# Kernel optimization log

Measured on AMD Instinct MI355X. Metric: run time of the kernel, lower is better.

## Reference

```python
import jax, jax.numpy as jnp
import numpy as np

B, N, D, H, F = 16, 257, 1024, 16, 4096
HD = D // H
EPS = 1e-5
GATING_TEMP = 0.25  # gating_hyperparam for steep_sigmoid
SCALE = HD ** -0.5


def layer_norm(x, g, b):
    mu = jnp.mean(x, axis=-1, keepdims=True)
    var = jnp.mean(jnp.square(x - mu), axis=-1, keepdims=True)
    return (x - mu) * jax.lax.rsqrt(var + EPS) * g + b


def quick_gelu(x):
    return x * jax.nn.sigmoid(1.702 * x)


def setup_inputs() -> dict:
    key = jax.random.key(0)
    ks = jax.random.split(key, 24)
    s = 0.02
    inp = {
        'hidden_states': jax.random.normal(ks[0], (B, N, D), jnp.float32),
        'cached_hidden': jax.random.normal(ks[1], (B, N, D), jnp.float32),
        'cached_q': jax.random.normal(ks[2], (B, N, D), jnp.float32),
        'cached_k': jax.random.normal(ks[3], (B, N, D), jnp.float32),
        'cached_v': jax.random.normal(ks[4], (B, N, D), jnp.float32),
        'ln1_g': jnp.ones((D,), jnp.float32),
        'ln1_b': jnp.zeros((D,), jnp.float32),
        'wq': jax.random.normal(ks[5], (D, D), jnp.float32) * s,
        'bq': jnp.zeros((D,), jnp.float32),
        'wk': jax.random.normal(ks[6], (D, D), jnp.float32) * s,
        'bk': jnp.zeros((D,), jnp.float32),
        'wv': jax.random.normal(ks[7], (D, D), jnp.float32) * s,
        'bv': jnp.zeros((D,), jnp.float32),
        'wo': jax.random.normal(ks[8], (D, D), jnp.float32) * s,
        'bo': jnp.zeros((D,), jnp.float32),
        'ln2_g': jnp.ones((D,), jnp.float32),
        'ln2_b': jnp.zeros((D,), jnp.float32),
        'w1': jax.random.normal(ks[9], (D, F), jnp.float32) * s,
        'b1': jnp.zeros((F,), jnp.float32),
        'w2': jax.random.normal(ks[10], (F, D), jnp.float32) * s,
        'b2': jnp.zeros((D,), jnp.float32),
        'threshold': jnp.float32(0.5),
    }
    return inp


def reference(hidden_states, cached_hidden, cached_q, cached_k, cached_v,
              ln1_g, ln1_b, wq, bq, wk, bk, wv, bv, wo, bo,
              ln2_g, ln2_b, w1, b1, w2, b2, threshold):
    # layer_norm1 + QKV projection (layer_norm1_qkv_projection)
    h_ln = layer_norm(hidden_states, ln1_g, ln1_b)
    q = h_ln @ wq + bq
    k = h_ln @ wk + bk
    v = h_ln @ wv + bv

    # reuse module: cosine^1 similarity vs cached hidden, steep_sigmoid gating
    # against learned threshold; soft gather/scatter blend of cached states.
    num = jnp.sum(cached_hidden * hidden_states, axis=-1)           # [B,N]
    den = (jnp.linalg.norm(cached_hidden, axis=-1)
           * jnp.linalg.norm(hidden_states, axis=-1) + 1e-8)
    sim = num / den                                                 # [B,N]
    gate = jax.nn.sigmoid((sim - threshold) / GATING_TEMP)[..., None]  # [B,N,1]

    hidden = gate * cached_hidden + (1.0 - gate) * hidden_states
    q = gate * cached_q + (1.0 - gate) * q
    k = gate * cached_k + (1.0 - gate) * k
    v = gate * cached_v + (1.0 - gate) * v

    # manual bmm-softmax-bmm attention
    qh = (q * SCALE).reshape(B, N, H, HD).transpose(0, 2, 1, 3)  # [B,H,N,hd]
    kh = k.reshape(B, N, H, HD).transpose(0, 2, 1, 3)
    vh = v.reshape(B, N, H, HD).transpose(0, 2, 1, 3)
    scores = jnp.einsum('bhqd,bhkd->bhqk', qh, kh)
    probs = jax.nn.softmax(scores, axis=-1)
    attn = jnp.einsum('bhqk,bhkd->bhqd', probs, vh)
    attn = attn.transpose(0, 2, 1, 3).reshape(B, N, D)
    attn = attn @ wo + bo

    hidden = hidden + attn
    residual = hidden
    hidden = layer_norm(hidden, ln2_g, ln2_b)
    hidden = quick_gelu(hidden @ w1 + b1) @ w2 + b2
    return residual + hidden
```

## Files before the change

### kernel.cpp

```cpp
#include <hip/hip_runtime.h>
#include <hip/hip_bf16.h>
#include <stdint.h>

#define BB   16
#define SEQ  257
#define DD   1024
#define NH   16
#define HD_  64
#define FF   4096
#define MM   (BB*SEQ)
#define MPAD2 4352
#define SPAD 272
#define VPAD 288
#define SCALE_Q 0.125f

typedef __bf16 bf16x8 __attribute__((ext_vector_type(8)));
typedef float  f32x4  __attribute__((ext_vector_type(4)));
typedef unsigned short u16;

__device__ __forceinline__ u16 f2bf(float f) {
  uint32_t u = __float_as_uint(f);
  uint32_t r = (u + 0x7FFFu + ((u >> 16) & 1u)) >> 16;
  return (u16)r;
}
__device__ __forceinline__ float bf2f(u16 u) {
  return __uint_as_float(((uint32_t)u) << 16);
}
__device__ __forceinline__ void gll16(const void* g, void* l) {
  __builtin_amdgcn_global_load_lds(
      (const __attribute__((address_space(1))) void*)g,
      (__attribute__((address_space(3))) void*)l, 16, 0, 0);
}
__device__ __forceinline__ float wsum(float v) {
  #pragma unroll
  for (int o = 1; o < 64; o <<= 1) v += __shfl_xor(v, o);
  return v;
}

__global__ __launch_bounds__(256) void transpose_all(
    const float* __restrict__ wq, const float* __restrict__ wk,
    const float* __restrict__ wv, const float* __restrict__ wo,
    const float* __restrict__ w1, const float* __restrict__ w2,
    u16* __restrict__ wqkvT, u16* __restrict__ woT,
    u16* __restrict__ w1T, u16* __restrict__ w2T) {
  __shared__ float tile[64][65];
  const int bid = blockIdx.x;
  const float* src;  u16* dst;  int R, C, b;
  if (bid < 768)       { int s = bid >> 8;  b = bid & 255;
                         src = s==0?wq:(s==1?wk:wv);  dst = wqkvT + s*1024*1024;
                         R = 1024; C = 1024; }
  else if (bid < 1024) { src = wo;  dst = woT;  b = bid - 768;   R = 1024; C = 1024; }
  else if (bid < 2048) { src = w1;  dst = w1T;  b = bid - 1024;  R = 1024; C = 4096; }
  else                 { src = w2;  dst = w2T;  b = bid - 2048;  R = 4096; C = 1024; }
  const int ctiles = C >> 6;
  const int r0 = (b / ctiles) << 6, c0 = (b % ctiles) << 6;
  const int tx = threadIdx.x & 63, ty = threadIdx.x >> 6;
  #pragma unroll
  for (int it = 0; it < 16; ++it) {
    int rr = it * 4 + ty;
    tile[rr][tx] = src[(size_t)(r0 + rr) * C + c0 + tx];
  }
  __syncthreads();
  #pragma unroll
  for (int it = 0; it < 16; ++it) {
    int rr = it * 4 + ty;
    dst[(size_t)(c0 + rr) * R + r0 + tx] = f2bf(tile[tx][rr]);
  }
}

__global__ __launch_bounds__(256) void vtrans_kernel(
    const u16* __restrict__ vb, u16* __restrict__ vt) {
  __shared__ u16 tile[64][72];
  const int bh = blockIdx.x, c = blockIdx.y;
  const int tx = threadIdx.x & 63, ty = threadIdx.x >> 6;
  const u16* src = vb + (size_t)bh * SPAD * HD_;
  u16* dst = vt + (size_t)bh * HD_ * VPAD;
  #pragma unroll
  for (int it = 0; it < 16; ++it) {
    int r = it * 4 + ty;
    int nn = c * 64 + r;  int nnc = nn < SPAD ? nn : SPAD - 1;
    tile[r][tx] = src[(size_t)nnc * HD_ + tx];
  }
  __syncthreads();
  #pragma unroll
  for (int it = 0; it < 16; ++it) {
    int hd = it * 4 + ty;
    int col = c * 64 + tx;
    if (col < VPAD) dst[(size_t)hd * VPAD + col] = tile[tx][hd];
  }
}

__global__ __launch_bounds__(256) void ln1_gate_kernel(
    const float* __restrict__ h, const float* __restrict__ c,
    const float* __restrict__ g, const float* __restrict__ bta,
    const float* __restrict__ thr, u16* __restrict__ hln,
    float* __restrict__ hblend, float* __restrict__ gate) {
  int m = blockIdx.x, t = threadIdx.x, l = t & 63, w = t >> 6;
  const float4 hv = *(const float4*)(h + (size_t)m * DD + t * 4);
  const float4 cv = *(const float4*)(c + (size_t)m * DD + t * 4);
  float sh = hv.x + hv.y + hv.z + hv.w;
  float sh2 = hv.x*hv.x + hv.y*hv.y + hv.z*hv.z + hv.w*hv.w;
  float sch = hv.x*cv.x + hv.y*cv.y + hv.z*cv.z + hv.w*cv.w;
  float sc2 = cv.x*cv.x + cv.y*cv.y + cv.z*cv.z + cv.w*cv.w;
  sh = wsum(sh); sh2 = wsum(sh2); sch = wsum(sch); sc2 = wsum(sc2);
  __shared__ float red[4][4];
  if (l == 0) { red[w][0]=sh; red[w][1]=sh2; red[w][2]=sch; red[w][3]=sc2; }
  __syncthreads();
  float Sh  = red[0][0]+red[1][0]+red[2][0]+red[3][0];
  float Sh2 = red[0][1]+red[1][1]+red[2][1]+red[3][1];
  float Sch = red[0][2]+red[1][2]+red[2][2]+red[3][2];
  float Sc2 = red[0][3]+red[1][3]+red[2][3]+red[3][3];
  float mean = Sh * (1.f/DD);
  float var  = Sh2 * (1.f/DD) - mean*mean;
  float rs   = rsqrtf(var + 1e-5f);
  float sim  = Sch / (sqrtf(Sc2)*sqrtf(Sh2) + 1e-8f);
  float gv   = 1.f / (1.f + __expf(-(sim - thr[0]) * 4.0f));
  float4 gg = *(const float4*)(g + t*4);
  float4 bb = *(const float4*)(bta + t*4);
  ushort4 ob;
  ob.x = f2bf((hv.x-mean)*rs*gg.x + bb.x);
  ob.y = f2bf((hv.y-mean)*rs*gg.y + bb.y);
  ob.z = f2bf((hv.z-mean)*rs*gg.z + bb.z);
  ob.w = f2bf((hv.w-mean)*rs*gg.w + bb.w);
  *(ushort4*)(hln + (size_t)m * DD + t * 4) = ob;
  float4 hb;
  hb.x = gv*cv.x + (1.f-gv)*hv.x;  hb.y = gv*cv.y + (1.f-gv)*hv.y;
  hb.z = gv*cv.z + (1.f-gv)*hv.z;  hb.w = gv*cv.w + (1.f-gv)*hv.w;
  *(float4*)(hblend + (size_t)m * DD + t * 4) = hb;
  if (t == 0) gate[m] = gv;
}

__global__ __launch_bounds__(256) void ln2_kernel(
    const float* __restrict__ in, const float* __restrict__ g,
    const float* __restrict__ bta, u16* __restrict__ outb) {
  int m = blockIdx.x, t = threadIdx.x, l = t & 63, w = t >> 6;
  const float4 hv = *(const float4*)(in + (size_t)m * DD + t * 4);
  float sh = hv.x + hv.y + hv.z + hv.w;
  float sh2 = hv.x*hv.x + hv.y*hv.y + hv.z*hv.z + hv.w*hv.w;
  sh = wsum(sh); sh2 = wsum(sh2);
  __shared__ float red[4][2];
  if (l == 0) { red[w][0] = sh; red[w][1] = sh2; }
  __syncthreads();
  float Sh  = red[0][0]+red[1][0]+red[2][0]+red[3][0];
  float Sh2 = red[0][1]+red[1][1]+red[2][1]+red[3][1];
  float mean = Sh * (1.f/DD);
  float rs = rsqrtf(Sh2 * (1.f/DD) - mean*mean + 1e-5f);
  float4 gg = *(const float4*)(g + t*4);
  float4 bb = *(const float4*)(bta + t*4);
  ushort4 ob;
  ob.x = f2bf((hv.x-mean)*rs*gg.x + bb.x);
  ob.y = f2bf((hv.y-mean)*rs*gg.y + bb.y);
  ob.z = f2bf((hv.z-mean)*rs*gg.z + bb.z);
  ob.w = f2bf((hv.w-mean)*rs*gg.w + bb.w);
  *(ushort4*)(outb + (size_t)m * DD + t * 4) = ob;
}

template<int EPI>
__global__ __launch_bounds__(256) void gemm_bt(
    const u16* __restrict__ A, const u16* __restrict__ Bt,
    int Kstride, int Kiter,
    const float* __restrict__ bias,
    const float* __restrict__ gate,
    const float* __restrict__ c0, const float* __restrict__ c1, const float* __restrict__ c2,
    const float* __restrict__ bq, const float* __restrict__ bk, const float* __restrict__ bv,
    u16* __restrict__ qb, u16* __restrict__ kb, u16* __restrict__ vb,
    const float* __restrict__ addsrc, float* __restrict__ outf,
    u16* __restrict__ outb, u16* __restrict__ partb) {
  const int tid = threadIdx.x, w = tid >> 6, l = tid & 63, lr = l & 15, lh = l >> 4;
  const int Mt = gridDim.x;
  const int f = blockIdx.y * Mt + blockIdx.x;
  const int nwg = Mt * gridDim.y;
  const int swz = (f & 7) * (nwg >> 3) + (f >> 3);
  const int m0 = (swz % Mt) * 128, n0 = (swz / Mt) * 128;
  const int kBase = blockIdx.z * Kiter;
  const int wm = w >> 1, wn = w & 1;
  __shared__ u16 sA[2][4096], sB[2][4096];
  f32x4 acc[4][4];
  f32x4 zero = {0.f, 0.f, 0.f, 0.f};
  #pragma unroll
  for (int i = 0; i < 4; ++i)
    #pragma unroll
    for (int j = 0; j < 4; ++j) acc[i][j] = zero;

  const int r0 = tid >> 2, cc = (tid & 3) * 8;
  const u16* ga0 = A  + (size_t)(m0 + r0) * Kstride + kBase + cc;
  const u16* ga1 = A  + (size_t)(m0 + 64 + r0) * Kstride + kBase + cc;
  const u16* gb0 = Bt + (size_t)(n0 + r0) * Kstride + kBase + cc;
  const u16* gb1 = Bt + (size_t)(n0 + 64 + r0) * Kstride + kBase + cc;

  const int nt = Kiter >> 5;
  gll16(ga0, &sA[0][w*512]);  gll16(ga1, &sA[0][2048 + w*512]);
  gll16(gb0, &sB[0][w*512]);  gll16(gb1, &sB[0][2048 + w*512]);

  for (int t = 0; t < nt; ++t) {
    const int cur = t & 1;
    __syncthreads();
    if (t + 1 < nt) {
      const int k0 = (t + 1) << 5;
      gll16(ga0 + k0, &sA[cur^1][w*512]);  gll16(ga1 + k0, &sA[cur^1][2048 + w*512]);
      gll16(gb0 + k0, &sB[cur^1][w*512]);  gll16(gb1 + k0, &sB[cur^1][2048 + w*512]);
    }
    bf16x8 af[4], bfr[4];
    #pragma unroll
    for (int mi = 0; mi < 4; ++mi)
      af[mi] = *(const bf16x8*)&sA[cur][(wm*64 + mi*16 + lr)*32 + lh*8];
    #pragma unroll
    for (int ni = 0; ni < 4; ++ni)
      bfr[ni] = *(const bf16x8*)&sB[cur][(wn*64 + ni*16 + lr)*32 + lh*8];
    #pragma unroll
    for (int mi = 0; mi < 4; ++mi)
      #pragma unroll
      for (int ni = 0; ni < 4; ++ni)
        acc[mi][ni] = __builtin_amdgcn_mfma_f32_16x16x32_bf16(af[mi], bfr[ni], acc[mi][ni], 0, 0, 0);
  }

  if constexpr (EPI == 0) {
    const int which = n0 >> 10;
    const float* cb = which==0 ? bq : (which==1 ? bk : bv);
    const float* cp = which==0 ? c0 : (which==1 ? c1 : c2);
    u16* dst = which==0 ? qb : (which==1 ? kb : vb);
    const float scl = which==0 ? SCALE_Q : 1.0f;
    #pragma unroll
    for (int mi = 0; mi < 4; ++mi) {
      #pragma unroll
      for (int r = 0; r < 4; ++r) {
        const int row = m0 + wm*64 + mi*16 + lh*4 + r;
        if (row < MM) {
          const float gv = gate[row];
          const int bidx = row / SEQ, nn = row - bidx * SEQ;
          #pragma unroll
          for (int ni = 0; ni < 4; ++ni) {
            const int col = n0 + wn*64 + ni*16 + lr;
            const int d = col & 1023, hd = d & 63, hh = d >> 6;
            const float lin = acc[mi][ni][r] + cb[d];
            const float val = (gv * cp[(size_t)row*DD + d] + (1.f - gv) * lin) * scl;
            dst[((size_t)(bidx*NH + hh)*SPAD + nn)*HD_ + hd] = f2bf(val);
          }
        }
      }
    }
  } else if constexpr (EPI == 1) {
    #pragma unroll
    for (int mi = 0; mi < 4; ++mi)
      #pragma unroll
      for (int r = 0; r < 4; ++r) {
        const int row = m0 + wm*64 + mi*16 + lh*4 + r;
        if (row < MM) {
          #pragma unroll
          for (int ni = 0; ni < 4; ++ni) {
            const int col = n0 + wn*64 + ni*16 + lr;
            outf[(size_t)row*DD + col] = acc[mi][ni][r] + bias[col] + addsrc[(size_t)row*DD + col];
          }
        }
      }
  } else if constexpr (EPI == 2) {
    #pragma unroll
    for (int mi = 0; mi < 4; ++mi)
      #pragma unroll
      for (int r = 0; r < 4; ++r) {
        const int row = m0 + wm*64 + mi*16 + lh*4 + r;
        if (row < MM) {
          #pragma unroll
          for (int ni = 0; ni < 4; ++ni) {
            const int col = n0 + wn*64 + ni*16 + lr;
            const float x = acc[mi][ni][r] + bias[col];
            const float s = 1.f / (1.f + __expf(-1.702f * x));
            outb[(size_t)row*FF + col] = f2bf(x * s);
          }
        }
      }
  } else {
    u16* pp = partb + (size_t)blockIdx.z * ((size_t)MPAD2 * 1024);
    #pragma unroll
    for (int mi = 0; mi < 4; ++mi)
      #pragma unroll
      for (int r = 0; r < 4; ++r) {
        const int row = m0 + wm*64 + mi*16 + lh*4 + r;
        if (row < MM) {
          #pragma unroll
          for (int ni = 0; ni < 4; ++ni) {
            const int col = n0 + wn*64 + ni*16 + lr;
            pp[(size_t)row*1024 + col] = f2bf(acc[mi][ni][r]);
          }
        }
      }
  }
}

__global__ __launch_bounds__(256) void reduce_mlp2(
    const u16* __restrict__ parts, const float* __restrict__ bias,
    const float* __restrict__ resid, float* __restrict__ out) {
  const size_t PS = (size_t)MPAD2 * 1024;
  const int row = blockIdx.x, t = threadIdx.x, c = t * 4;
  const size_t base = (size_t)row * 1024 + c;
  float4 r = *(const float4*)(resid + base);
  float4 b = *(const float4*)(bias + c);
  float o0 = r.x + b.x, o1 = r.y + b.y, o2 = r.z + b.z, o3 = r.w + b.w;
  #pragma unroll
  for (int p = 0; p < 2; ++p) {
    ushort4 u = *(const ushort4*)(parts + p*PS + base);
    o0 += bf2f(u.x);  o1 += bf2f(u.y);  o2 += bf2f(u.z);  o3 += bf2f(u.w);
  }
  float4 o;  o.x = o0;  o.y = o1;  o.z = o2;  o.w = o3;
  *(float4*)(out + base) = o;
}

__global__ __launch_bounds__(256) void attn_kernel(
    const u16* __restrict__ qb, const u16* __restrict__ kb,
    const u16* __restrict__ vt, u16* __restrict__ attn_out) {
  __shared__ u16 P[64 * 296];
  const int bh = blockIdx.x, b = bh >> 4, hh = bh & 15;
  const int q0 = blockIdx.y * 64;
  const int tid = threadIdx.x, w = tid >> 6, l = tid & 63, lr = l & 15, lh = l >> 4;
  const u16* qp = qb + (size_t)bh * SPAD * HD_;
  const u16* kp = kb + (size_t)bh * SPAD * HD_;
  const u16* vp = vt + (size_t)bh * HD_ * VPAD;

  const int qr = q0 + w*16 + lr;
  const int qrc = qr < 271 ? qr : 271;
  bf16x8 aq0 = *(const bf16x8*)(qp + (size_t)qrc*HD_ + lh*8);
  bf16x8 aq1 = *(const bf16x8*)(qp + (size_t)qrc*HD_ + 32 + lh*8);

  f32x4 st[18];
  f32x4 zero = {0.f,0.f,0.f,0.f};
  #pragma unroll
  for (int t = 0; t < 18; ++t) st[t] = zero;
  #pragma unroll
  for (int t = 0; t < 18; ++t) {
    int key = t*16 + lr;  int keyc = key < 271 ? key : 271;
    bf16x8 b0 = *(const bf16x8*)(kp + (size_t)keyc*HD_ + lh*8);
    bf16x8 b1 = *(const bf16x8*)(kp + (size_t)keyc*HD_ + 32 + lh*8);
    st[t] = __builtin_amdgcn_mfma_f32_16x16x32_bf16(aq0, b0, st[t], 0, 0, 0);
    st[t] = __builtin_amdgcn_mfma_f32_16x16x32_bf16(aq1, b1, st[t], 0, 0, 0);
  }
  #pragma unroll
  for (int t = 0; t < 18; ++t) {
    int key = t*16 + lr;
    if (key >= SEQ) { st[t][0]=-1e30f; st[t][1]=-1e30f; st[t][2]=-1e30f; st[t][3]=-1e30f; }
  }
  float mr[4], sr[4];
  #pragma unroll
  for (int r = 0; r < 4; ++r) {
    float m = st[0][r];
    #pragma unroll
    for (int t = 1; t < 18; ++t) m = fmaxf(m, st[t][r]);
    m = fmaxf(m, __shfl_xor(m, 1));  m = fmaxf(m, __shfl_xor(m, 2));
    m = fmaxf(m, __shfl_xor(m, 4));  m = fmaxf(m, __shfl_xor(m, 8));
    mr[r] = m;  sr[r] = 0.f;
  }
  #pragma unroll
  for (int t = 0; t < 18; ++t)
    #pragma unroll
    for (int r = 0; r < 4; ++r) {
      float p = __expf(st[t][r] - mr[r]);
      st[t][r] = p;  sr[r] += p;
    }
  #pragma unroll
  for (int r = 0; r < 4; ++r) {
    sr[r] += __shfl_xor(sr[r], 1);  sr[r] += __shfl_xor(sr[r], 2);
    sr[r] += __shfl_xor(sr[r], 4);  sr[r] += __shfl_xor(sr[r], 8);
  }
  #pragma unroll
  for (int t = 0; t < 18; ++t)
    #pragma unroll
    for (int r = 0; r < 4; ++r)
      P[(w*16 + lh*4 + r)*296 + t*16 + lr] = f2bf(st[t][r]);
  __syncthreads();

  f32x4 o[4];
  #pragma unroll
  for (int ni = 0; ni < 4; ++ni) o[ni] = zero;
  #pragma unroll
  for (int ks = 0; ks < 9; ++ks) {
    bf16x8 pa = *(const bf16x8*)&P[(w*16 + lr)*296 + ks*32 + lh*8];
    #pragma unroll
    for (int ni = 0; ni < 4; ++ni) {
      bf16x8 bv_ = *(const bf16x8*)(vp + (size_t)(ni*16 + lr)*VPAD + ks*32 + lh*8);
      o[ni] = __builtin_amdgcn_mfma_f32_16x16x32_bf16(pa, bv_, o[ni], 0, 0, 0);
    }
  }
  #pragma unroll
  for (int r = 0; r < 4; ++r) {
    const int qrow = q0 + w*16 + lh*4 + r;
    if (qrow < SEQ) {
      const float inv = 1.f / sr[r];
      #pragma unroll
      for (int ni = 0; ni < 4; ++ni)
        attn_out[(size_t)(b*SEQ + qrow)*DD + hh*HD_ + ni*16 + lr] = f2bf(o[ni][r] * inv);
    }
  }
}

extern "C" void kernel_launch(void* const* d_in, const int* in_sizes, int n_in,
                              void* d_out, int out_size, void* d_ws, size_t ws_size,
                              hipStream_t stream) {
  (void)in_sizes; (void)n_in; (void)out_size; (void)ws_size;
  const float* hidden   = (const float*)d_in[0];
  const float* cached_h = (const float*)d_in[1];
  const float* cached_q = (const float*)d_in[2];
  const float* cached_k = (const float*)d_in[3];
  const float* cached_v = (const float*)d_in[4];
  const float* ln1_g = (const float*)d_in[5];
  const float* ln1_b = (const float*)d_in[6];
  const float* wq = (const float*)d_in[7];
  const float* bq = (const float*)d_in[8];
  const float* wk = (const float*)d_in[9];
  const float* bk = (const float*)d_in[10];
  const float* wv = (const float*)d_in[11];
  const float* bv = (const float*)d_in[12];
  const float* wo = (const float*)d_in[13];
  const float* bo = (const float*)d_in[14];
  const float* ln2_g = (const float*)d_in[15];
  const float* ln2_b = (const float*)d_in[16];
  const float* w1 = (const float*)d_in[17];
  const float* b1 = (const float*)d_in[18];
  const float* w2 = (const float*)d_in[19];
  const float* b2 = (const float*)d_in[20];
  const float* thr = (const float*)d_in[21];
  float* out = (float*)d_out;

  char* ws = (char*)d_ws;
  size_t off = 0;
  auto alloc = [&](size_t bytes) {
    void* p = ws + off;  off += (bytes + 255) & ~(size_t)255;  return p;
  };
  u16*   wqkvT  = (u16*)alloc(3072ull * 1024 * 2);
  u16*   woT    = (u16*)alloc(1024ull * 1024 * 2);
  u16*   w1T    = (u16*)alloc(4096ull * 1024 * 2);
  u16*   w2T    = (u16*)alloc(1024ull * 4096 * 2);
  float* gate   = (float*)alloc((size_t)MPAD2 * 4);
  float* resid2 = (float*)alloc((size_t)MPAD2 * DD * 4);
  u16*   regA   = (u16*)alloc((size_t)MPAD2 * DD * 2);
  u16 *hln = regA, *attn_o = regA, *ln2out = regA;
  const size_t QKV_B  = (size_t)256 * SPAD * HD_ * 2;
  const size_t VT_B   = (size_t)256 * HD_ * VPAD * 2;
  const size_t PART_B = (size_t)MPAD2 * 1024 * 2;
  const size_t partsOff = 3*QKV_B + VT_B;
  char*  regB   = (char*)alloc(partsOff + 2*PART_B);
  u16*   qbuf   = (u16*)regB;
  u16*   kbuf   = (u16*)(regB + QKV_B);
  u16*   vbuf   = (u16*)(regB + 2*QKV_B);
  u16*   vtb    = (u16*)(regB + 3*QKV_B);
  float* hblend = (float*)(regB + partsOff);
  u16*   mid    = (u16*)regB;
  u16*   parts  = (u16*)(regB + partsOff);

  dim3 blk(256);
  transpose_all<<<dim3(3072), blk, 0, stream>>>(wq, wk, wv, wo, w1, w2,
                                                wqkvT, woT, w1T, w2T);

  ln1_gate_kernel<<<dim3(MM), blk, 0, stream>>>(hidden, cached_h, ln1_g, ln1_b, thr,
                                                hln, hblend, gate);

  gemm_bt<0><<<dim3(33, 24), blk, 0, stream>>>(hln, wqkvT, 1024, 1024, nullptr,
      gate, cached_q, cached_k, cached_v, bq, bk, bv, qbuf, kbuf, vbuf,
      nullptr, nullptr, nullptr, nullptr);

  vtrans_kernel<<<dim3(256, 5), blk, 0, stream>>>(vbuf, vtb);
  attn_kernel<<<dim3(256, 5), blk, 0, stream>>>(qbuf, kbuf, vtb, attn_o);

  gemm_bt<1><<<dim3(33, 8), blk, 0, stream>>>(attn_o, woT, 1024, 1024, bo,
      nullptr, nullptr, nullptr, nullptr, nullptr, nullptr, nullptr,
      nullptr, nullptr, nullptr, hblend, resid2, nullptr, nullptr);

  ln2_kernel<<<dim3(MM), blk, 0, stream>>>(resid2, ln2_g, ln2_b, ln2out);

  gemm_bt<2><<<dim3(33, 32), blk, 0, stream>>>(ln2out, w1T, 1024, 1024, b1,
      nullptr, nullptr, nullptr, nullptr, nullptr, nullptr, nullptr,
      nullptr, nullptr, nullptr, nullptr, nullptr, mid, nullptr);

  gemm_bt<3><<<dim3(33, 8, 2), blk, 0, stream>>>(mid, w2T, 4096, 2048, nullptr,
      nullptr, nullptr, nullptr, nullptr, nullptr, nullptr, nullptr,
      nullptr, nullptr, nullptr, nullptr, nullptr, nullptr, parts);

  reduce_mlp2<<<dim3(MM), blk, 0, stream>>>(parts, b2, resid2, out);
}
```

Measured before the change: 313.5 us.

## Double GEMM K-tile to 64 with XOR-swizzled LDS layout

```diff
diff --git a/kernel.cpp b/kernel.cpp
--- a/kernel.cpp
+++ b/kernel.cpp
@@ -174,7 +174,7 @@
   const int m0 = (swz % Mt) * 128, n0 = (swz / Mt) * 128;
   const int kBase = blockIdx.z * Kiter;
   const int wm = w >> 1, wn = w & 1;
-  __shared__ u16 sA[2][4096], sB[2][4096];
+  __shared__ u16 sA[2][8192], sB[2][8192];
   f32x4 acc[4][4];
   f32x4 zero = {0.f, 0.f, 0.f, 0.f};
   #pragma unroll
@@ -182,37 +182,48 @@
     #pragma unroll
     for (int j = 0; j < 4; ++j) acc[i][j] = zero;
 
-  const int r0 = tid >> 2, cc = (tid & 3) * 8;
-  const u16* ga0 = A  + (size_t)(m0 + r0) * Kstride + kBase + cc;
-  const u16* ga1 = A  + (size_t)(m0 + 64 + r0) * Kstride + kBase + cc;
-  const u16* gb0 = Bt + (size_t)(n0 + r0) * Kstride + kBase + cc;
-  const u16* gb1 = Bt + (size_t)(n0 + 64 + r0) * Kstride + kBase + cc;
-
-  const int nt = Kiter >> 5;
-  gll16(ga0, &sA[0][w*512]);  gll16(ga1, &sA[0][2048 + w*512]);
-  gll16(gb0, &sB[0][w*512]);  gll16(gb1, &sB[0][2048 + w*512]);
-
+  const int rS = tid >> 3;
+  const int srcC = ((tid & 7) ^ (rS & 7)) * 8;
+  const u16* gA = A  + (size_t)(m0 + rS) * Kstride + kBase + srcC;
+  const u16* gB = Bt + (size_t)(n0 + rS) * Kstride + kBase + srcC;
+  const size_t rStep = (size_t)32 * Kstride;
+
+  const int rdA = (wm*64 + lr) * 64;
+  const int rdB = (wn*64 + lr) * 64;
+  const int cx0 = ((lh ^ (lr & 7)) & 7) * 8;
+
+  #define STAGE(BUF_, T_) do { \
+    const int _ko = (T_) * 64; \
+    _Pragma("unroll") \
+    for (int _j = 0; _j < 4; ++_j) { \
+      gll16(gA + _ko + _j*rStep, &sA[BUF_][_j*2048] + tid*8); \
+      gll16(gB + _ko + _j*rStep, &sB[BUF_][_j*2048] + tid*8); \
+    } } while(0)
+
+  const int nt = Kiter >> 6;
+  STAGE(0, 0);
   for (int t = 0; t < nt; ++t) {
     const int cur = t & 1;
     __syncthreads();
-    if (t + 1 < nt) {
-      const int k0 = (t + 1) << 5;
-      gll16(ga0 + k0, &sA[cur^1][w*512]);  gll16(ga1 + k0, &sA[cur^1][2048 + w*512]);
-      gll16(gb0 + k0, &sB[cur^1][w*512]);  gll16(gb1 + k0, &sB[cur^1][2048 + w*512]);
+    if (t + 1 < nt) STAGE(cur ^ 1, t + 1);
+    #pragma unroll
+    for (int ks = 0; ks < 2; ++ks) {
+      const int co = cx0 ^ (ks * 32);
+      bf16x8 af[4], bfr[4];
+      #pragma unroll
+      for (int mi = 0; mi < 4; ++mi)
+        af[mi] = *(const bf16x8*)&sA[cur][rdA + mi*1024 + co];
+      #pragma unroll
+      for (int ni = 0; ni < 4; ++ni)
+        bfr[ni] = *(const bf16x8*)&sB[cur][rdB + ni*1024 + co];
+      #pragma unroll
+      for (int mi = 0; mi < 4; ++mi)
+        #pragma unroll
+        for (int ni = 0; ni < 4; ++ni)
+          acc[mi][ni] = __builtin_amdgcn_mfma_f32_16x16x32_bf16(af[mi], bfr[ni], acc[mi][ni], 0, 0, 0);
     }
-    bf16x8 af[4], bfr[4];
-    #pragma unroll
-    for (int mi = 0; mi < 4; ++mi)
-      af[mi] = *(const bf16x8*)&sA[cur][(wm*64 + mi*16 + lr)*32 + lh*8];
-    #pragma unroll
-    for (int ni = 0; ni < 4; ++ni)
-      bfr[ni] = *(const bf16x8*)&sB[cur][(wn*64 + ni*16 + lr)*32 + lh*8];
-    #pragma unroll
-    for (int mi = 0; mi < 4; ++mi)
-      #pragma unroll
-      for (int ni = 0; ni < 4; ++ni)
-        acc[mi][ni] = __builtin_amdgcn_mfma_f32_16x16x32_bf16(af[mi], bfr[ni], acc[mi][ni], 0, 0, 0);
-  }
+  }
+  #undef STAGE
 
   if constexpr (EPI == 0) {
     const int which = n0 >> 10;
```

New measurement: 308.2 us. No clear change (-1.7%).

## Triple-buffer GEMM LDS pipeline with XOR-swizzled layout and remainder-aware XCD swizzle

Applied to the files above, without the earlier changes.

```diff
diff --git a/kernel.cpp b/kernel.cpp
--- a/kernel.cpp
+++ b/kernel.cpp
@@ -156,7 +156,7 @@
 }
 
 template<int EPI>
-__global__ __launch_bounds__(256) void gemm_bt(
+__global__ __launch_bounds__(256, 3) void gemm_bt(
     const u16* __restrict__ A, const u16* __restrict__ Bt,
     int Kstride, int Kiter,
     const float* __restrict__ bias,
@@ -170,11 +170,12 @@
   const int Mt = gridDim.x;
   const int f = blockIdx.y * Mt + blockIdx.x;
   const int nwg = Mt * gridDim.y;
-  const int swz = (f & 7) * (nwg >> 3) + (f >> 3);
+  const int q8 = nwg >> 3, r8 = nwg & 7, xcd = f & 7, lin = f >> 3;
+  const int swz = (xcd < r8 ? xcd * (q8 + 1) : r8 * (q8 + 1) + (xcd - r8) * q8) + lin;
   const int m0 = (swz % Mt) * 128, n0 = (swz / Mt) * 128;
   const int kBase = blockIdx.z * Kiter;
   const int wm = w >> 1, wn = w & 1;
-  __shared__ u16 sA[2][4096], sB[2][4096];
+  __shared__ u16 sA[3][4096], sB[3][4096];
   f32x4 acc[4][4];
   f32x4 zero = {0.f, 0.f, 0.f, 0.f};
   #pragma unroll
@@ -182,37 +183,57 @@
     #pragma unroll
     for (int j = 0; j < 4; ++j) acc[i][j] = zero;
 
-  const int r0 = tid >> 2, cc = (tid & 3) * 8;
-  const u16* ga0 = A  + (size_t)(m0 + r0) * Kstride + kBase + cc;
-  const u16* ga1 = A  + (size_t)(m0 + 64 + r0) * Kstride + kBase + cc;
-  const u16* gb0 = Bt + (size_t)(n0 + r0) * Kstride + kBase + cc;
-  const u16* gb1 = Bt + (size_t)(n0 + 64 + r0) * Kstride + kBase + cc;
+  const int rS = tid >> 2;
+  const int srcC = (((tid & 3) ^ ((tid >> 3) & 3)) * 8);
+  const u16* gA = A  + (size_t)(m0 + rS) * Kstride + kBase + srcC;
+  const u16* gB = Bt + (size_t)(n0 + rS) * Kstride + kBase + srcC;
+  const size_t rStep = (size_t)64 * Kstride;
+
+  const int sL = (lr >> 1) & 3;
+  const int coff = ((lh ^ sL) & 3) * 8;
+  const int rdA = (wm*64 + lr) * 32 + coff;
+  const int rdB = (wn*64 + lr) * 32 + coff;
+
+  #define STAGE(S_, T_) do { \
+    const int _ko = (T_) << 5; \
+    gll16(gA + _ko,         &sA[S_][0]    + tid*8); \
+    gll16(gA + _ko + rStep, &sA[S_][2048] + tid*8); \
+    gll16(gB + _ko,         &sB[S_][0]    + tid*8); \
+    gll16(gB + _ko + rStep, &sB[S_][2048] + tid*8); \
+  } while(0)
 
   const int nt = Kiter >> 5;
-  gll16(ga0, &sA[0][w*512]);  gll16(ga1, &sA[0][2048 + w*512]);
-  gll16(gb0, &sB[0][w*512]);  gll16(gb1, &sB[0][2048 + w*512]);
-
+  STAGE(0, 0);
+  STAGE(1, 1);
+  #pragma unroll 1
   for (int t = 0; t < nt; ++t) {
-    const int cur = t & 1;
-    __syncthreads();
-    if (t + 1 < nt) {
-      const int k0 = (t + 1) << 5;
-      gll16(ga0 + k0, &sA[cur^1][w*512]);  gll16(ga1 + k0, &sA[cur^1][2048 + w*512]);
-      gll16(gb0 + k0, &sB[cur^1][w*512]);  gll16(gb1 + k0, &sB[cur^1][2048 + w*512]);
+    const int sc = t % 3;
+    __builtin_amdgcn_s_barrier();
+    if (t + 2 < nt) {
+      STAGE((t + 2) % 3, t + 2);
+      asm volatile("s_waitcnt vmcnt(8)" ::: "memory");
+    } else if (t + 1 < nt) {
+      asm volatile("s_waitcnt vmcnt(4)" ::: "memory");
+    } else {
+      asm volatile("s_waitcnt vmcnt(0)" ::: "memory");
     }
+    __builtin_amdgcn_sched_barrier(0);
+    __builtin_amdgcn_s_barrier();
+    __builtin_amdgcn_sched_barrier(0);
     bf16x8 af[4], bfr[4];
     #pragma unroll
     for (int mi = 0; mi < 4; ++mi)
-      af[mi] = *(const bf16x8*)&sA[cur][(wm*64 + mi*16 + lr)*32 + lh*8];
+      af[mi] = *(const bf16x8*)&sA[sc][rdA + mi*512];
     #pragma unroll
     for (int ni = 0; ni < 4; ++ni)
-      bfr[ni] = *(const bf16x8*)&sB[cur][(wn*64 + ni*16 + lr)*32 + lh*8];
+      bfr[ni] = *(const bf16x8*)&sB[sc][rdB + ni*512];
     #pragma unroll
     for (int mi = 0; mi < 4; ++mi)
       #pragma unroll
       for (int ni = 0; ni < 4; ++ni)
         acc[mi][ni] = __builtin_amdgcn_mfma_f32_16x16x32_bf16(af[mi], bfr[ni], acc[mi][ni], 0, 0, 0);
   }
+  #undef STAGE
 
   if constexpr (EPI == 0) {
     const int which = n0 >> 10;
@@ -232,8 +253,8 @@
           for (int ni = 0; ni < 4; ++ni) {
             const int col = n0 + wn*64 + ni*16 + lr;
             const int d = col & 1023, hd = d & 63, hh = d >> 6;
-            const float lin = acc[mi][ni][r] + cb[d];
-            const float val = (gv * cp[(size_t)row*DD + d] + (1.f - gv) * lin) * scl;
+            const float lin2 = acc[mi][ni][r] + cb[d];
+            const float val = (gv * cp[(size_t)row*DD + d] + (1.f - gv) * lin2) * scl;
             dst[((size_t)(bidx*NH + hh)*SPAD + nn)*HD_ + hd] = f2bf(val);
           }
         }
```

Result: no change. 313.1 us (-0.1%).
